# Optimization experiments

Hardware: AMD Instinct MI355X
Metric: run time of the kernel (lower is better)

The kernel has to match this reference:

```python
import jax, jax.numpy as jnp
import numpy as np

H = 768


def _glorot(key, shape):
    fan_in = shape[-1]
    return jax.random.normal(key, shape, dtype=jnp.float32) / np.sqrt(fan_in)


def setup_inputs() -> dict:
    key = jax.random.key(0)
    ks = jax.random.split(key, 12)
    B, L, K, Lg = 8, 256, 32, 128
    return {
        "x": jax.random.normal(ks[0], (B, L, H), dtype=jnp.float32),
        "s": jax.random.normal(ks[1], (B, K, H), dtype=jnp.float32),
        "g": jax.random.normal(ks[2], (B, Lg, H), dtype=jnp.float32),
        "Wq": _glorot(ks[3], (H, H)),
        "bq": jnp.zeros((H,), jnp.float32),
        "Wkv": _glorot(ks[4], (2 * H, H)),
        "bkv": jnp.zeros((2 * H,), jnp.float32),
        "Wg1": _glorot(ks[5], (H, 2 * H)),
        "bg1": jnp.zeros((H,), jnp.float32),
        "Wg2": _glorot(ks[6], (H, 2 * H)),
        "bg2": jnp.zeros((H,), jnp.float32),
    }


def _gate(xb, yb, W, b):
    # gate = sigmoid(Linear(concat([x, y], -1))) using split-weight trick:
    # concat([x,y]) @ W.T = x @ Wx.T + y @ Wy.T  (avoids materializing 2H concat)
    Wx, Wy = W[:, :H], W[:, H:]
    gate = jax.nn.sigmoid(jnp.einsum('blkh,oh->blko', xb, Wx)
                          + jnp.einsum('blkh,oh->blko', yb, Wy) + b)
    return gate * xb + (1.0 - gate) * yb


def reference(x, s, g, Wq, bq, Wkv, bkv, Wg1, bg1, Wg2, bg2):
    B, L, _ = x.shape
    K = s.shape[1]
    q = jnp.einsum('blh,oh->blo', x, Wq) + bq                    # (B,L,H)
    kv = jnp.einsum('bmh,oh->bmo', g, Wkv) + bkv                 # (B,Lg,2H)
    k, v = kv[..., :H], kv[..., H:]
    scores = jnp.einsum('blh,bmh->blm', q, k) / np.sqrt(H)       # (B,L,Lg)
    scores = jax.nn.softmax(scores, axis=-1)
    gctx = jnp.einsum('blm,bmh->blh', scores, v)                 # (B,L,H)
    # broadcast to (B,L,K,H)
    gb = jnp.broadcast_to(gctx[:, :, None, :], (B, L, K, H))
    hb = jnp.broadcast_to(x[:, :, None, :], (B, L, K, H))
    sb = jnp.broadcast_to(s[:, None, :, :], (B, L, K, H))
    h = _gate(hb, gb, Wg1, bg1)
    h = _gate(h, sb, Wg2, bg2)
    return h
```

## Files before the change

kernel.cpp:

```cpp
#include <hip/hip_runtime.h>
#include <math.h>

#define Hd 768
#define Bb 8
#define Ll 256
#define Kk 32
#define LG 128

using half4 = __attribute__((ext_vector_type(4))) _Float16;
using half8 = __attribute__((ext_vector_type(8))) _Float16;
using f32x4 = __attribute__((ext_vector_type(4))) float;

__device__ __forceinline__ float sigm(float z) { return 1.f / (1.f + __expf(-z)); }

struct ConvArgs {
    const float* src[8];
    _Float16*    dst[8];
    int cum[9];
    int sstr[8];
    int dstr[8];
    int rl[8];
};

__global__ __launch_bounds__(256) void conv_multi(ConvArgs a) {
    int c = blockIdx.x * 256 + threadIdx.x;
    if (c >= a.cum[8]) return;
    int s = 0;
    while (c >= a.cum[s + 1]) ++s;
    const int lc  = c - a.cum[s];
    const unsigned cpr = (unsigned)(a.rl[s] >> 3);
    const unsigned row = (unsigned)lc / cpr;
    const int col = (lc - (int)(row * cpr)) * 8;
    const float* sp = a.src[s] + (size_t)row * a.sstr[s] + col;
    float4 v0 = *(const float4*)sp;
    float4 v1 = *(const float4*)(sp + 4);
    half8 h;
    h[0] = (_Float16)v0.x; h[1] = (_Float16)v0.y; h[2] = (_Float16)v0.z; h[3] = (_Float16)v0.w;
    h[4] = (_Float16)v1.x; h[5] = (_Float16)v1.y; h[6] = (_Float16)v1.z; h[7] = (_Float16)v1.w;
    *(half8*)(a.dst[s] + (size_t)row * a.dstr[s] + col) = h;
}


struct G3Desc {
    const _Float16* A;
    const _Float16* W;
    const float* bias;
    void* o0;
    void* o1;
    int lda, ldw, mode, nbx;
};
struct G3Args { G3Desc d[3]; int cum[4]; };

__global__ __launch_bounds__(256) void gemm3(G3Args ga) {
    __shared__ _Float16 As[64][72];
    __shared__ _Float16 Ws[64][72];

    const int t    = threadIdx.x;
    const int w    = t >> 6;
    const int lane = t & 63;
    const int quad = lane >> 4;
    const int l16  = lane & 15;

    int s = 0;
    const int bid = blockIdx.x;
    while (bid >= ga.cum[s + 1]) ++s;
    const int local = bid - ga.cum[s];
    const int nbx   = ga.d[s].nbx;
    const int by    = local / nbx;
    const int bx    = local - by * nbx;
    const int bm    = by * 64;
    const int bn    = bx * 64;
    const _Float16* A = ga.d[s].A;
    const _Float16* W = ga.d[s].W;
    const int lda = ga.d[s].lda;
    const int ldw = ga.d[s].ldw;

    const int sr = t >> 3;
    const int sk = (t & 7) * 8;

    f32x4 acc[4] = {};

    half8 av[2], wv[2];
    #pragma unroll
    for (int i = 0; i < 2; ++i) {
        av[i] = *(const half8*)(A + (size_t)(bm + i * 32 + sr) * lda + sk);
        wv[i] = *(const half8*)(W + (size_t)(bn + i * 32 + sr) * ldw + sk);
    }

    for (int k0 = 0; k0 < 768; k0 += 64) {
        __syncthreads();
        #pragma unroll
        for (int i = 0; i < 2; ++i) {
            *(half8*)&As[i * 32 + sr][sk] = av[i];
            *(half8*)&Ws[i * 32 + sr][sk] = wv[i];
        }
        __syncthreads();
        if (k0 + 64 < 768) {
            #pragma unroll
            for (int i = 0; i < 2; ++i) {
                av[i] = *(const half8*)(A + (size_t)(bm + i * 32 + sr) * lda + k0 + 64 + sk);
                wv[i] = *(const half8*)(W + (size_t)(bn + i * 32 + sr) * ldw + k0 + 64 + sk);
            }
        }
        __builtin_amdgcn_sched_barrier(0);
        #pragma unroll
        for (int kk = 0; kk < 2; ++kk) {
            half8 af = *(const half8*)&As[w * 16 + l16][kk * 32 + quad * 8];
            #pragma unroll
            for (int j = 0; j < 4; ++j) {
                half8 bf = *(const half8*)&Ws[j * 16 + l16][kk * 32 + quad * 8];
                acc[j] = __builtin_amdgcn_mfma_f32_16x16x32_f16(af, bf, acc[j], 0, 0, 0);
            }
        }
    }

    const int mode = ga.d[s].mode;
    const float* bias = ga.d[s].bias;
    #pragma unroll
    for (int j = 0; j < 4; ++j) {
        const int col  = bn + j * 16 + l16;
        const int row0 = bm + w * 16 + quad * 4;
        const float bv = bias ? bias[col] : 0.f;
        if (mode == 0) {
            _Float16* C2 = (_Float16*)ga.d[s].o0;
            #pragma unroll
            for (int r = 0; r < 4; ++r)
                C2[(size_t)(row0 + r) * 768 + col] = (_Float16)(acc[j][r] + bv);
        } else if (mode == 1) {
            _Float16* K16  = (_Float16*)ga.d[s].o0;
            _Float16* VT16 = (_Float16*)ga.d[s].o1;
            if (col < 768) {
                #pragma unroll
                for (int r = 0; r < 4; ++r)
                    K16[(size_t)(row0 + r) * 768 + col] = (_Float16)(acc[j][r] + bv);
            } else {
                const int b = row0 >> 7, h = col - 768, m0 = row0 & 127;
                half4 hv;
                #pragma unroll
                for (int r = 0; r < 4; ++r) hv[r] = (_Float16)(acc[j][r] + bv);
                *(half4*)(VT16 + ((size_t)(b * 768 + h)) * 128 + m0) = hv;
            }
        } else {
            float* C = (float*)ga.d[s].o0;
            #pragma unroll
            for (int r = 0; r < 4; ++r)
                C[(size_t)(row0 + r) * 768 + col] = acc[j][r] + bv;
        }
    }
}

__global__ __launch_bounds__(256) void attn_scores_sm(
    const _Float16* __restrict__ Q, const _Float16* __restrict__ Kt,
    _Float16* __restrict__ P)
{
    __shared__ _Float16 As[64][72];
    __shared__ _Float16 Ws[128][72];

    const int t    = threadIdx.x;
    const int w    = t >> 6;
    const int lane = t & 63;
    const int quad = lane >> 4;
    const int l16  = lane & 15;
    const int z    = blockIdx.y;
    const int bm   = blockIdx.x * 64;
    const _Float16* A = Q  + (size_t)z * 256 * 768 + (size_t)bm * 768;
    const _Float16* W = Kt + (size_t)z * 128 * 768;

    const int sr = t >> 3;
    const int sk = (t & 7) * 8;

    f32x4 acc[8] = {};

    half8 av[2], wv[4];
    #pragma unroll
    for (int i = 0; i < 2; ++i)
        av[i] = *(const half8*)(A + (size_t)(i * 32 + sr) * 768 + sk);
    #pragma unroll
    for (int i = 0; i < 4; ++i)
        wv[i] = *(const half8*)(W + (size_t)(i * 32 + sr) * 768 + sk);

    for (int k0 = 0; k0 < 768; k0 += 64) {
        __syncthreads();
        #pragma unroll
        for (int i = 0; i < 2; ++i) *(half8*)&As[i * 32 + sr][sk] = av[i];
        #pragma unroll
        for (int i = 0; i < 4; ++i) *(half8*)&Ws[i * 32 + sr][sk] = wv[i];
        __syncthreads();
        if (k0 + 64 < 768) {
            #pragma unroll
            for (int i = 0; i < 2; ++i)
                av[i] = *(const half8*)(A + (size_t)(i * 32 + sr) * 768 + k0 + 64 + sk);
            #pragma unroll
            for (int i = 0; i < 4; ++i)
                wv[i] = *(const half8*)(W + (size_t)(i * 32 + sr) * 768 + k0 + 64 + sk);
        }
        __builtin_amdgcn_sched_barrier(0);
        #pragma unroll
        for (int kk = 0; kk < 2; ++kk) {
            half8 af = *(const half8*)&As[w * 16 + l16][kk * 32 + quad * 8];
            #pragma unroll
            for (int j = 0; j < 8; ++j) {
                half8 bf = *(const half8*)&Ws[j * 16 + l16][kk * 32 + quad * 8];
                acc[j] = __builtin_amdgcn_mfma_f32_16x16x32_f16(af, bf, acc[j], 0, 0, 0);
            }
        }
    }

    const float scale = 0.03608439182435161f;
    #pragma unroll
    for (int r = 0; r < 4; ++r) {
        float v[8];
        float mx = -1e30f;
        #pragma unroll
        for (int j = 0; j < 8; ++j) { v[j] = acc[j][r] * scale; mx = fmaxf(mx, v[j]); }
        #pragma unroll
        for (int off = 8; off; off >>= 1) mx = fmaxf(mx, __shfl_xor(mx, off, 16));
        float sum = 0.f;
        #pragma unroll
        for (int j = 0; j < 8; ++j) { v[j] = __expf(v[j] - mx); sum += v[j]; }
        #pragma unroll
        for (int off = 8; off; off >>= 1) sum += __shfl_xor(sum, off, 16);
        const float inv = 1.f / sum;
        const int row = bm + w * 16 + quad * 4 + r;
        _Float16* Pr = P + (size_t)z * 256 * 128 + (size_t)row * 128;
        #pragma unroll
        for (int j = 0; j < 8; ++j) Pr[j * 16 + l16] = (_Float16)(v[j] * inv);
    }
}

__global__ __launch_bounds__(256) void gemm_gctx(
    const _Float16* __restrict__ A, int lda, long sA,
    const _Float16* __restrict__ W, int ldw, long sW,
    float* __restrict__ C, int ldc, long sC,
    _Float16* __restrict__ C2, int ldc2, long sC2)
{
    __shared__ _Float16 As[64][72];
    __shared__ _Float16 Ws[64][72];

    const int t    = threadIdx.x;
    const int w    = t >> 6;
    const int lane = t & 63;
    const int quad = lane >> 4;
    const int l16  = lane & 15;
    const int bm   = blockIdx.y * 64;
    const int bn   = blockIdx.x * 64;
    const int z    = blockIdx.z;
    A += (size_t)z * sA;
    W += (size_t)z * sW;

    const int sr = t >> 3;
    const int sk = (t & 7) * 8;

    f32x4 acc[4] = {};

    half8 av[2], wv[2];
    #pragma unroll
    for (int i = 0; i < 2; ++i) {
        av[i] = *(const half8*)(A + (size_t)(bm + i * 32 + sr) * lda + sk);
        wv[i] = *(const half8*)(W + (size_t)(bn + i * 32 + sr) * ldw + sk);
    }

    for (int k0 = 0; k0 < 128; k0 += 64) {
        __syncthreads();
        #pragma unroll
        for (int i = 0; i < 2; ++i) {
            *(half8*)&As[i * 32 + sr][sk] = av[i];
            *(half8*)&Ws[i * 32 + sr][sk] = wv[i];
        }
        __syncthreads();
        if (k0 + 64 < 128) {
            #pragma unroll
            for (int i = 0; i < 2; ++i) {
                av[i] = *(const half8*)(A + (size_t)(bm + i * 32 + sr) * lda + k0 + 64 + sk);
                wv[i] = *(const half8*)(W + (size_t)(bn + i * 32 + sr) * ldw + k0 + 64 + sk);
            }
        }
        __builtin_amdgcn_sched_barrier(0);
        #pragma unroll
        for (int kk = 0; kk < 2; ++kk) {
            half8 af = *(const half8*)&As[w * 16 + l16][kk * 32 + quad * 8];
            #pragma unroll
            for (int j = 0; j < 4; ++j) {
                half8 bf = *(const half8*)&Ws[j * 16 + l16][kk * 32 + quad * 8];
                acc[j] = __builtin_amdgcn_mfma_f32_16x16x32_f16(af, bf, acc[j], 0, 0, 0);
            }
        }
    }

    #pragma unroll
    for (int j = 0; j < 4; ++j) {
        const int col  = bn + j * 16 + l16;
        const int row0 = bm + w * 16 + quad * 4;
        #pragma unroll
        for (int r = 0; r < 4; ++r) {
            const float v = acc[j][r];
            const size_t rr = (size_t)(row0 + r);
            C[(size_t)z * sC + rr * ldc + col] = v;
            C2[(size_t)z * sC2 + rr * ldc2 + col] = (_Float16)v;
        }
    }
}

__global__ __launch_bounds__(256) void gemm_gate1(
    const _Float16* __restrict__ A,
    const _Float16* __restrict__ W,
    const float* __restrict__ bias,
    const float* __restrict__ X,
    const float* __restrict__ GC,
    float* __restrict__ H1,
    _Float16* __restrict__ H16)
{
    __shared__ _Float16 As[64][72];
    __shared__ _Float16 Ws[64][72];

    const int t    = threadIdx.x;
    const int w    = t >> 6;
    const int lane = t & 63;
    const int quad = lane >> 4;
    const int l16  = lane & 15;
    const int bm   = blockIdx.y * 64;
    const int bn   = blockIdx.x * 64;

    const int sr = t >> 3;
    const int sk = (t & 7) * 8;

    f32x4 acc[4] = {};

    half8 av[2], wv[2];
    #pragma unroll
    for (int i = 0; i < 2; ++i) {
        av[i] = *(const half8*)(A + (size_t)(bm + i * 32 + sr) * 1536 + sk);
        wv[i] = *(const half8*)(W + (size_t)(bn + i * 32 + sr) * 1536 + sk);
    }

    for (int k0 = 0; k0 < 1536; k0 += 64) {
        __syncthreads();
        #pragma unroll
        for (int i = 0; i < 2; ++i) {
            *(half8*)&As[i * 32 + sr][sk] = av[i];
            *(half8*)&Ws[i * 32 + sr][sk] = wv[i];
        }
        __syncthreads();
        if (k0 + 64 < 1536) {
            #pragma unroll
            for (int i = 0; i < 2; ++i) {
                av[i] = *(const half8*)(A + (size_t)(bm + i * 32 + sr) * 1536 + k0 + 64 + sk);
                wv[i] = *(const half8*)(W + (size_t)(bn + i * 32 + sr) * 1536 + k0 + 64 + sk);
            }
        }
        __builtin_amdgcn_sched_barrier(0);
        #pragma unroll
        for (int kk = 0; kk < 2; ++kk) {
            half8 af = *(const half8*)&As[w * 16 + l16][kk * 32 + quad * 8];
            #pragma unroll
            for (int j = 0; j < 4; ++j) {
                half8 bf = *(const half8*)&Ws[j * 16 + l16][kk * 32 + quad * 8];
                acc[j] = __builtin_amdgcn_mfma_f32_16x16x32_f16(af, bf, acc[j], 0, 0, 0);
            }
        }
    }

    #pragma unroll
    for (int j = 0; j < 4; ++j) {
        const int col  = bn + j * 16 + l16;
        const int row0 = bm + w * 16 + quad * 4;
        const float bv = bias[col];
        #pragma unroll
        for (int r = 0; r < 4; ++r) {
            const size_t off = (size_t)(row0 + r) * 768 + col;
            const float g = sigm(acc[j][r] + bv);
            const float o = g * X[off] + (1.f - g) * GC[off];
            H1[off]  = o;
            H16[off] = (_Float16)o;
        }
    }
}

__global__ __launch_bounds__(256) void gemm_final(
    const _Float16* __restrict__ A,
    const _Float16* __restrict__ W,
    const float* __restrict__ bias,
    const float* __restrict__ Ebuf,
    const float* __restrict__ Sbuf,
    const float* __restrict__ H1,
    float* __restrict__ out)
{
    __shared__ union {
        struct { _Float16 As[64][72]; _Float16 Ws[64][72]; } a;
        float Ds[64][76];
    } u;
    __shared__ float Es[32][64];
    __shared__ float Ss[32][64];

    const int t    = threadIdx.x;
    const int w    = t >> 6;
    const int lane = t & 63;
    const int quad = lane >> 4;
    const int l16  = lane & 15;
    const int bm   = blockIdx.y * 64;
    const int bn   = blockIdx.x * 64;
    const int bK   = (bm >> 8) * 32;

    const int sr = t >> 3;
    const int sk = (t & 7) * 8;

    #pragma unroll
    for (int i = 0; i < 2; ++i) {
        const int idx = t + i * 256;
        const int k = idx >> 4, c = (idx & 15) * 4;
        *(float4*)&Es[k][c] = *(const float4*)(Ebuf + (size_t)(bK + k) * 768 + bn + c);
        *(float4*)&Ss[k][c] = *(const float4*)(Sbuf + (size_t)(bK + k) * 768 + bn + c);
    }

    f32x4 acc[4] = {};

    half8 av[2], wv[2];
    #pragma unroll
    for (int i = 0; i < 2; ++i) {
        av[i] = *(const half8*)(A + (size_t)(bm + i * 32 + sr) * 768 + sk);
        wv[i] = *(const half8*)(W + (size_t)(bn + i * 32 + sr) * 768 + sk);
    }

    for (int k0 = 0; k0 < 768; k0 += 64) {
        __syncthreads();
        #pragma unroll
        for (int i = 0; i < 2; ++i) {
            *(half8*)&u.a.As[i * 32 + sr][sk] = av[i];
            *(half8*)&u.a.Ws[i * 32 + sr][sk] = wv[i];
        }
        __syncthreads();
        if (k0 + 64 < 768) {
            #pragma unroll
            for (int i = 0; i < 2; ++i) {
                av[i] = *(const half8*)(A + (size_t)(bm + i * 32 + sr) * 768 + k0 + 64 + sk);
                wv[i] = *(const half8*)(W + (size_t)(bn + i * 32 + sr) * 768 + k0 + 64 + sk);
            }
        }
        __builtin_amdgcn_sched_barrier(0);
        #pragma unroll
        for (int kk = 0; kk < 2; ++kk) {
            half8 af = *(const half8*)&u.a.As[w * 16 + l16][kk * 32 + quad * 8];
            #pragma unroll
            for (int j = 0; j < 4; ++j) {
                half8 bf = *(const half8*)&u.a.Ws[j * 16 + l16][kk * 32 + quad * 8];
                acc[j] = __builtin_amdgcn_mfma_f32_16x16x32_f16(af, bf, acc[j], 0, 0, 0);
            }
        }
    }

    __syncthreads();
    #pragma unroll
    for (int j = 0; j < 4; ++j) {
        const int col = j * 16 + l16;
        const float bv = bias[bn + col];
        #pragma unroll
        for (int r = 0; r < 4; ++r)
            u.Ds[w * 16 + quad * 4 + r][col] = acc[j][r] + bv;
    }
    __syncthreads();

    const int c  = (t & 15) * 4;
    const int r0 = (t >> 4) * 4;
    float4 d[4], h[4];
    #pragma unroll
    for (int rr = 0; rr < 4; ++rr) {
        d[rr] = *(const float4*)&u.Ds[r0 + rr][c];
        h[rr] = *(const float4*)(H1 + (size_t)(bm + r0 + rr) * 768 + bn + c);
    }
    float* ob = out + (size_t)(bm + r0) * 32 * 768 + bn + c;
    for (int k = 0; k < 32; ++k) {
        const float4 e  = *(const float4*)&Es[k][c];
        const float4 sv = *(const float4*)&Ss[k][c];
        #pragma unroll
        for (int rr = 0; rr < 4; ++rr) {
            float4 o; float g;
            g = sigm(d[rr].x + e.x); o.x = g * h[rr].x + (1.f - g) * sv.x;
            g = sigm(d[rr].y + e.y); o.y = g * h[rr].y + (1.f - g) * sv.y;
            g = sigm(d[rr].z + e.z); o.z = g * h[rr].z + (1.f - g) * sv.z;
            g = sigm(d[rr].w + e.w); o.w = g * h[rr].w + (1.f - g) * sv.w;
            *(float4*)(ob + (size_t)(rr * 32 + k) * 768) = o;
        }
    }
}

extern "C" void kernel_launch(void* const* d_in, const int* in_sizes, int n_in,
                              void* d_out, int out_size, void* d_ws, size_t ws_size,
                              hipStream_t stream) {
    const float* x   = (const float*)d_in[0];
    const float* s   = (const float*)d_in[1];
    const float* g   = (const float*)d_in[2];
    const float* Wq  = (const float*)d_in[3];
    const float* bq  = (const float*)d_in[4];
    const float* Wkv = (const float*)d_in[5];
    const float* bkv = (const float*)d_in[6];
    const float* Wg1 = (const float*)d_in[7];
    const float* bg1 = (const float*)d_in[8];
    const float* Wg2 = (const float*)d_in[9];
    const float* bg2 = (const float*)d_in[10];

    char* w = (char*)d_ws;
    _Float16* P16    = (_Float16*)(w + 0);
    _Float16* xg16   = (_Float16*)(w + 524288);
    _Float16* g16    = (_Float16*)(w + 6815744);
    _Float16* s16    = (_Float16*)(w + 8388608);
    _Float16* q16    = (_Float16*)(w + 8781824);
    _Float16* k16    = (_Float16*)(w + 11927552);
    _Float16* vT16   = (_Float16*)(w + 13500416);
    _Float16* Wq16   = (_Float16*)(w + 15073280);
    _Float16* Wkv16  = (_Float16*)(w + 16252928);
    _Float16* Wg116  = (_Float16*)(w + 18612224);
    _Float16* Wg2a16 = (_Float16*)(w + 20971520);
    _Float16* Wg2b16 = (_Float16*)(w + 22151168);
    float*    bufE   = (float*)(w + 23330816);
    float*    bufC   = (float*)(w + 24117248);
    float*    bufB   = (float*)(w + 30408704);
    _Float16* h116   = (_Float16*)(w + 36700160);
    float* out = (float*)d_out;

    const dim3 blk(256);

    ConvArgs ca;
    ca.src[0] = x;         ca.dst[0] = xg16;   ca.sstr[0] = 768;  ca.dstr[0] = 1536; ca.rl[0] = 768;
    ca.src[1] = g;         ca.dst[1] = g16;    ca.sstr[1] = 768;  ca.dstr[1] = 768;  ca.rl[1] = 768;
    ca.src[2] = s;         ca.dst[2] = s16;    ca.sstr[2] = 768;  ca.dstr[2] = 768;  ca.rl[2] = 768;
    ca.src[3] = Wq;        ca.dst[3] = Wq16;   ca.sstr[3] = 768;  ca.dstr[3] = 768;  ca.rl[3] = 768;
    ca.src[4] = Wkv;       ca.dst[4] = Wkv16;  ca.sstr[4] = 768;  ca.dstr[4] = 768;  ca.rl[4] = 768;
    ca.src[5] = Wg1;       ca.dst[5] = Wg116;  ca.sstr[5] = 1536; ca.dstr[5] = 1536; ca.rl[5] = 1536;
    ca.src[6] = Wg2;       ca.dst[6] = Wg2a16; ca.sstr[6] = 1536; ca.dstr[6] = 768;  ca.rl[6] = 768;
    ca.src[7] = Wg2 + 768; ca.dst[7] = Wg2b16; ca.sstr[7] = 1536; ca.dstr[7] = 768;  ca.rl[7] = 768;
    ca.cum[0] = 0;      ca.cum[1] = 196608; ca.cum[2] = 294912; ca.cum[3] = 319488;
    ca.cum[4] = 393216; ca.cum[5] = 540672; ca.cum[6] = 688128; ca.cum[7] = 761856;
    ca.cum[8] = 835584;
    conv_multi<<<dim3(3264), blk, 0, stream>>>(ca);

    G3Args ga = {};
    ga.d[0] = { xg16, Wq16,   bq,      (void*)q16,  nullptr,     1536, 768, 0, 12 };
    ga.d[1] = { g16,  Wkv16,  bkv,     (void*)k16,  (void*)vT16, 768,  768, 1, 24 };
    ga.d[2] = { s16,  Wg2b16, nullptr, (void*)bufE, nullptr,     768,  768, 2, 12 };
    ga.cum[0] = 0; ga.cum[1] = 384; ga.cum[2] = 768; ga.cum[3] = 816;
    gemm3<<<dim3(816), blk, 0, stream>>>(ga);

    attn_scores_sm<<<dim3(4, 8), blk, 0, stream>>>(q16, k16, P16);

    gemm_gctx<<<dim3(12, 4, 8), blk, 0, stream>>>(
        P16, 128, 256L * 128, vT16, 128, 768L * 128,
        bufC, 768, 256L * 768, xg16 + 768, 1536, 256L * 1536);

    gemm_gate1<<<dim3(12, 32), blk, 0, stream>>>(
        xg16, Wg116, bg1, x, bufC, bufB, h116);

    gemm_final<<<dim3(12, 32), blk, 0, stream>>>(
        h116, Wg2a16, bg2, bufE, s, bufB, out);
}
```

Before: 311.4 us.

## Fuse all stages into one persistent cooperative kernel with grid syncs

Replaces the six separate launches (conversion, batched projection GEMMs, attention scores, P·V, gate1, final gate) with one cooperative persistent kernel of 512 blocks. Stages are separated by grid.sync() and share a union of shared-memory layouts. The attention stage now fuses softmax with P·V in-block, so the P matrix never goes to global memory. This removes launch gaps and the P round-trip. In exchange, the attention stage runs on only 32 blocks while the rest idle, grid-wide barriers add their own cost, and the larger shared footprint with 2-block occupancy may limit overlap.

```diff
diff --git a/kernel.cpp b/kernel.cpp
--- a/kernel.cpp
+++ b/kernel.cpp
@@ -1,11 +1,10 @@
 #include <hip/hip_runtime.h>
+#include <hip/hip_cooperative_groups.h>
 #include <math.h>
 
-#define Hd 768
-#define Bb 8
-#define Ll 256
-#define Kk 32
-#define LG 128
+namespace cg = cooperative_groups;
+
+#define NBLK 512
 
 using half4 = __attribute__((ext_vector_type(4))) _Float16;
 using half8 = __attribute__((ext_vector_type(8))) _Float16;
@@ -21,25 +20,6 @@
     int dstr[8];
     int rl[8];
 };
-
-__global__ __launch_bounds__(256) void conv_multi(ConvArgs a) {
-    int c = blockIdx.x * 256 + threadIdx.x;
-    if (c >= a.cum[8]) return;
-    int s = 0;
-    while (c >= a.cum[s + 1]) ++s;
-    const int lc  = c - a.cum[s];
-    const unsigned cpr = (unsigned)(a.rl[s] >> 3);
-    const unsigned row = (unsigned)lc / cpr;
-    const int col = (lc - (int)(row * cpr)) * 8;
-    const float* sp = a.src[s] + (size_t)row * a.sstr[s] + col;
-    float4 v0 = *(const float4*)sp;
-    float4 v1 = *(const float4*)(sp + 4);
-    half8 h;
-    h[0] = (_Float16)v0.x; h[1] = (_Float16)v0.y; h[2] = (_Float16)v0.z; h[3] = (_Float16)v0.w;
-    h[4] = (_Float16)v1.x; h[5] = (_Float16)v1.y; h[6] = (_Float16)v1.z; h[7] = (_Float16)v1.w;
-    *(half8*)(a.dst[s] + (size_t)row * a.dstr[s] + col) = h;
-}
-
 
 struct G3Desc {
     const _Float16* A;
@@ -51,434 +31,412 @@
 };
 struct G3Args { G3Desc d[3]; int cum[4]; };
 
-__global__ __launch_bounds__(256) void gemm3(G3Args ga) {
-    __shared__ _Float16 As[64][72];
-    __shared__ _Float16 Ws[64][72];
+struct FusedArgs {
+    ConvArgs ca;
+    G3Args   ga;
+    const _Float16* q16;
+    const _Float16* k16;
+    const _Float16* vT16;
+    float*          bufC;
+    _Float16*       xg16;
+    const _Float16* Wg116;
+    const float*    bg1;
+    const float*    x;
+    float*          bufB;
+    _Float16*       h116;
+    const _Float16* Wg2a16;
+    const float*    bg2;
+    const float*    bufE;
+    const float*    sIn;
+    float*          out;
+};
+
+union SharedAll {
+    struct { _Float16 As[64][72]; _Float16 Ws[64][72]; } g;
+    union {
+        struct { _Float16 As[64][72]; _Float16 Ws[128][72]; } qk;
+        struct { _Float16 Ps[64][136]; _Float16 Vs[64][136]; } pv;
+    } attn;
+    struct {
+        union { struct { _Float16 As[64][72]; _Float16 Ws[64][72]; } a;
+                float Ds[64][76]; } u;
+        float Es[32][64];
+        float Ss[32][64];
+    } fin;
+};
+
+__global__ __launch_bounds__(256, 2) void fused_all(FusedArgs fa) {
+    __shared__ SharedAll sh;
 
     const int t    = threadIdx.x;
     const int w    = t >> 6;
     const int lane = t & 63;
     const int quad = lane >> 4;
     const int l16  = lane & 15;
-
-    int s = 0;
-    const int bid = blockIdx.x;
-    while (bid >= ga.cum[s + 1]) ++s;
-    const int local = bid - ga.cum[s];
-    const int nbx   = ga.d[s].nbx;
-    const int by    = local / nbx;
-    const int bx    = local - by * nbx;
-    const int bm    = by * 64;
-    const int bn    = bx * 64;
-    const _Float16* A = ga.d[s].A;
-    const _Float16* W = ga.d[s].W;
-    const int lda = ga.d[s].lda;
-    const int ldw = ga.d[s].ldw;
-
-    const int sr = t >> 3;
-    const int sk = (t & 7) * 8;
-
-    f32x4 acc[4] = {};
-
-    half8 av[2], wv[2];
-    #pragma unroll
-    for (int i = 0; i < 2; ++i) {
-        av[i] = *(const half8*)(A + (size_t)(bm + i * 32 + sr) * lda + sk);
-        wv[i] = *(const half8*)(W + (size_t)(bn + i * 32 + sr) * ldw + sk);
+    const int sr   = t >> 3;
+    const int sk   = (t & 7) * 8;
+
+    cg::grid_group grid = cg::this_grid();
+
+    {
+        const ConvArgs& a = fa.ca;
+        for (int c = blockIdx.x * 256 + t; c < a.cum[8]; c += NBLK * 256) {
+            int seg = 0;
+            while (c >= a.cum[seg + 1]) ++seg;
+            const int lc  = c - a.cum[seg];
+            const unsigned cpr = (unsigned)(a.rl[seg] >> 3);
+            const unsigned row = (unsigned)lc / cpr;
+            const int col = (lc - (int)(row * cpr)) * 8;
+            const float* sp = a.src[seg] + (size_t)row * a.sstr[seg] + col;
+            float4 v0 = *(const float4*)sp;
+            float4 v1 = *(const float4*)(sp + 4);
+            half8 h;
+            h[0] = (_Float16)v0.x; h[1] = (_Float16)v0.y; h[2] = (_Float16)v0.z; h[3] = (_Float16)v0.w;
+            h[4] = (_Float16)v1.x; h[5] = (_Float16)v1.y; h[6] = (_Float16)v1.z; h[7] = (_Float16)v1.w;
+            *(half8*)(a.dst[seg] + (size_t)row * a.dstr[seg] + col) = h;
+        }
     }
-
-    for (int k0 = 0; k0 < 768; k0 += 64) {
+    grid.sync();
+
+    for (int bid = blockIdx.x; bid < 816; bid += NBLK) {
+        int seg = 0;
+        while (bid >= fa.ga.cum[seg + 1]) ++seg;
+        const G3Desc& d = fa.ga.d[seg];
+        const int local = bid - fa.ga.cum[seg];
+        const int by    = local / d.nbx;
+        const int bx    = local - by * d.nbx;
+        const int bm    = by * 64;
+        const int bn    = bx * 64;
+        const _Float16* A = d.A;
+        const _Float16* W = d.W;
+        const int lda = d.lda;
+        const int ldw = d.ldw;
+
+        f32x4 acc[4] = {};
+
+        half8 av[2], wv[2];
+        #pragma unroll
+        for (int i = 0; i < 2; ++i) {
+            av[i] = *(const half8*)(A + (size_t)(bm + i * 32 + sr) * lda + sk);
+            wv[i] = *(const half8*)(W + (size_t)(bn + i * 32 + sr) * ldw + sk);
+        }
+
+        for (int k0 = 0; k0 < 768; k0 += 64) {
+            __syncthreads();
+            #pragma unroll
+            for (int i = 0; i < 2; ++i) {
+                *(half8*)&sh.g.As[i * 32 + sr][sk] = av[i];
+                *(half8*)&sh.g.Ws[i * 32 + sr][sk] = wv[i];
+            }
+            __syncthreads();
+            if (k0 + 64 < 768) {
+                #pragma unroll
+                for (int i = 0; i < 2; ++i) {
+                    av[i] = *(const half8*)(A + (size_t)(bm + i * 32 + sr) * lda + k0 + 64 + sk);
+                    wv[i] = *(const half8*)(W + (size_t)(bn + i * 32 + sr) * ldw + k0 + 64 + sk);
+                }
+            }
+            __builtin_amdgcn_sched_barrier(0);
+            #pragma unroll
+            for (int kk = 0; kk < 2; ++kk) {
+                half8 af = *(const half8*)&sh.g.As[w * 16 + l16][kk * 32 + quad * 8];
+                #pragma unroll
+                for (int j = 0; j < 4; ++j) {
+                    half8 bf = *(const half8*)&sh.g.Ws[j * 16 + l16][kk * 32 + quad * 8];
+                    acc[j] = __builtin_amdgcn_mfma_f32_16x16x32_f16(af, bf, acc[j], 0, 0, 0);
+                }
+            }
+        }
+
+        const int mode = d.mode;
+        const float* bias = d.bias;
+        #pragma unroll
+        for (int j = 0; j < 4; ++j) {
+            const int col  = bn + j * 16 + l16;
+            const int row0 = bm + w * 16 + quad * 4;
+            const float bv = bias ? bias[col] : 0.f;
+            if (mode == 0) {
+                _Float16* C2 = (_Float16*)d.o0;
+                #pragma unroll
+                for (int r = 0; r < 4; ++r)
+                    C2[(size_t)(row0 + r) * 768 + col] = (_Float16)(acc[j][r] + bv);
+            } else if (mode == 1) {
+                _Float16* K16  = (_Float16*)d.o0;
+                _Float16* VT16 = (_Float16*)d.o1;
+                if (col < 768) {
+                    #pragma unroll
+                    for (int r = 0; r < 4; ++r)
+                        K16[(size_t)(row0 + r) * 768 + col] = (_Float16)(acc[j][r] + bv);
+                } else {
+                    const int b = row0 >> 7, h = col - 768, m0 = row0 & 127;
+                    half4 hv;
+                    #pragma unroll
+                    for (int r = 0; r < 4; ++r) hv[r] = (_Float16)(acc[j][r] + bv);
+                    *(half4*)(VT16 + ((size_t)(b * 768 + h)) * 128 + m0) = hv;
+                }
+            } else {
+                float* C = (float*)d.o0;
+                #pragma unroll
+                for (int r = 0; r < 4; ++r)
+                    C[(size_t)(row0 + r) * 768 + col] = acc[j][r] + bv;
+            }
+        }
+    }
+    grid.sync();
+
+    if (blockIdx.x < 32) {
+        const int z  = blockIdx.x >> 2;
+        const int bm = (blockIdx.x & 3) * 64;
+        const _Float16* A = fa.q16 + (size_t)z * 256 * 768 + (size_t)bm * 768;
+        const _Float16* W = fa.k16 + (size_t)z * 128 * 768;
+
+        f32x4 acc[8] = {};
+
+        half8 av[2], wv[4];
+        #pragma unroll
+        for (int i = 0; i < 2; ++i)
+            av[i] = *(const half8*)(A + (size_t)(i * 32 + sr) * 768 + sk);
+        #pragma unroll
+        for (int i = 0; i < 4; ++i)
+            wv[i] = *(const half8*)(W + (size_t)(i * 32 + sr) * 768 + sk);
+
+        for (int k0 = 0; k0 < 768; k0 += 64) {
+            __syncthreads();
+            #pragma unroll
+            for (int i = 0; i < 2; ++i) *(half8*)&sh.attn.qk.As[i * 32 + sr][sk] = av[i];
+            #pragma unroll
+            for (int i = 0; i < 4; ++i) *(half8*)&sh.attn.qk.Ws[i * 32 + sr][sk] = wv[i];
+            __syncthreads();
+            if (k0 + 64 < 768) {
+                #pragma unroll
+                for (int i = 0; i < 2; ++i)
+                    av[i] = *(const half8*)(A + (size_t)(i * 32 + sr) * 768 + k0 + 64 + sk);
+                #pragma unroll
+                for (int i = 0; i < 4; ++i)
+                    wv[i] = *(const half8*)(W + (size_t)(i * 32 + sr) * 768 + k0 + 64 + sk);
+            }
+            __builtin_amdgcn_sched_barrier(0);
+            #pragma unroll
+            for (int kk = 0; kk < 2; ++kk) {
+                half8 af = *(const half8*)&sh.attn.qk.As[w * 16 + l16][kk * 32 + quad * 8];
+                #pragma unroll
+                for (int j = 0; j < 8; ++j) {
+                    half8 bf = *(const half8*)&sh.attn.qk.Ws[j * 16 + l16][kk * 32 + quad * 8];
+                    acc[j] = __builtin_amdgcn_mfma_f32_16x16x32_f16(af, bf, acc[j], 0, 0, 0);
+                }
+            }
+        }
+
         __syncthreads();
+
+        const float scale = 0.03608439182435161f;
+        #pragma unroll
+        for (int r = 0; r < 4; ++r) {
+            float v[8];
+            float mx = -1e30f;
+            #pragma unroll
+            for (int j = 0; j < 8; ++j) { v[j] = acc[j][r] * scale; mx = fmaxf(mx, v[j]); }
+            #pragma unroll
+            for (int off = 8; off; off >>= 1) mx = fmaxf(mx, __shfl_xor(mx, off, 16));
+            float sum = 0.f;
+            #pragma unroll
+            for (int j = 0; j < 8; ++j) { v[j] = __expf(v[j] - mx); sum += v[j]; }
+            #pragma unroll
+            for (int off = 8; off; off >>= 1) sum += __shfl_xor(sum, off, 16);
+            const float inv = 1.f / sum;
+            const int prow = w * 16 + quad * 4 + r;
+            #pragma unroll
+            for (int j = 0; j < 8; ++j)
+                sh.attn.pv.Ps[prow][j * 16 + l16] = (_Float16)(v[j] * inv);
+        }
+
+        const _Float16* Vt = fa.vT16 + (size_t)z * 768 * 128;
+        float*     Cc = fa.bufC + ((size_t)(z * 256 + bm)) * 768;
+        _Float16*  Xg = fa.xg16 + ((size_t)(z * 256 + bm)) * 1536 + 768;
+
+        for (int cg = 0; cg < 12; ++cg) {
+            __syncthreads();
+            {
+                const int row = t >> 2;
+                const int cb  = (t & 3) * 32;
+                const _Float16* vp = Vt + (size_t)(cg * 64 + row) * 128 + cb;
+                *(half8*)&sh.attn.pv.Vs[row][cb]      = *(const half8*)(vp);
+                *(half8*)&sh.attn.pv.Vs[row][cb + 8]  = *(const half8*)(vp + 8);
+                *(half8*)&sh.attn.pv.Vs[row][cb + 16] = *(const half8*)(vp + 16);
+                *(half8*)&sh.attn.pv.Vs[row][cb + 24] = *(const half8*)(vp + 24);
+            }
+            __syncthreads();
+            f32x4 a2[4] = {};
+            #pragma unroll
+            for (int kk = 0; kk < 4; ++kk) {
+                half8 af = *(const half8*)&sh.attn.pv.Ps[w * 16 + l16][kk * 32 + quad * 8];
+                #pragma unroll
+                for (int j = 0; j < 4; ++j) {
+                    half8 bf = *(const half8*)&sh.attn.pv.Vs[j * 16 + l16][kk * 32 + quad * 8];
+                    a2[j] = __builtin_amdgcn_mfma_f32_16x16x32_f16(af, bf, a2[j], 0, 0, 0);
+                }
+            }
+            #pragma unroll
+            for (int j = 0; j < 4; ++j) {
+                const int col  = cg * 64 + j * 16 + l16;
+                const int row0 = w * 16 + quad * 4;
+                #pragma unroll
+                for (int r = 0; r < 4; ++r) {
+                    const float vv = a2[j][r];
+                    Cc[(size_t)(row0 + r) * 768 + col] = vv;
+                    Xg[(size_t)(row0 + r) * 1536 + col] = (_Float16)vv;
+                }
+            }
+        }
+    }
+    grid.sync();
+
+    for (int tile = blockIdx.x; tile < 384; tile += NBLK) {
+        const int by = tile / 12;
+        const int bx = tile - by * 12;
+        const int bm = by * 64;
+        const int bn = bx * 64;
+        const _Float16* A = fa.xg16;
+        const _Float16* W = fa.Wg116;
+
+        f32x4 acc[4] = {};
+
+        half8 av[2], wv[2];
         #pragma unroll
         for (int i = 0; i < 2; ++i) {
-            *(half8*)&As[i * 32 + sr][sk] = av[i];
-            *(half8*)&Ws[i * 32 + sr][sk] = wv[i];
-        }
+            av[i] = *(const half8*)(A + (size_t)(bm + i * 32 + sr) * 1536 + sk);
+            wv[i] = *(const half8*)(W + (size_t)(bn + i * 32 + sr) * 1536 + sk);
+        }
+
+        for (int k0 = 0; k0 < 1536; k0 += 64) {
+            __syncthreads();
+            #pragma unroll
+            for (int i = 0; i < 2; ++i) {
+                *(half8*)&sh.g.As[i * 32 + sr][sk] = av[i];
+                *(half8*)&sh.g.Ws[i * 32 + sr][sk] = wv[i];
+            }
+            __syncthreads();
+            if (k0 + 64 < 1536) {
+                #pragma unroll
+                for (int i = 0; i < 2; ++i) {
+                    av[i] = *(const half8*)(A + (size_t)(bm + i * 32 + sr) * 1536 + k0 + 64 + sk);
+                    wv[i] = *(const half8*)(W + (size_t)(bn + i * 32 + sr) * 1536 + k0 + 64 + sk);
+                }
+            }
+            __builtin_amdgcn_sched_barrier(0);
+            #pragma unroll
+            for (int kk = 0; kk < 2; ++kk) {
+                half8 af = *(const half8*)&sh.g.As[w * 16 + l16][kk * 32 + quad * 8];
+                #pragma unroll
+                for (int j = 0; j < 4; ++j) {
+                    half8 bf = *(const half8*)&sh.g.Ws[j * 16 + l16][kk * 32 + quad * 8];
+                    acc[j] = __builtin_amdgcn_mfma_f32_16x16x32_f16(af, bf, acc[j], 0, 0, 0);
+                }
+            }
+        }
+
+        #pragma unroll
+        for (int j = 0; j < 4; ++j) {
+            const int col  = bn + j * 16 + l16;
+            const int row0 = bm + w * 16 + quad * 4;
+            const float bv = fa.bg1[col];
+            #pragma unroll
+            for (int r = 0; r < 4; ++r) {
+                const size_t off = (size_t)(row0 + r) * 768 + col;
+                const float g = sigm(acc[j][r] + bv);
+                const float o = g * fa.x[off] + (1.f - g) * fa.bufC[off];
+                fa.bufB[off] = o;
+                fa.h116[off] = (_Float16)o;
+            }
+        }
+    }
+    grid.sync();
+
+    for (int tile = blockIdx.x; tile < 384; tile += NBLK) {
+        const int by = tile / 12;
+        const int bx = tile - by * 12;
+        const int bm = by * 64;
+        const int bn = bx * 64;
+        const int bK = (bm >> 8) * 32;
+        const _Float16* A = fa.h116;
+        const _Float16* W = fa.Wg2a16;
+
+        #pragma unroll
+        for (int i = 0; i < 2; ++i) {
+            const int idx = t + i * 256;
+            const int k = idx >> 4, c = (idx & 15) * 4;
+            *(float4*)&sh.fin.Es[k][c] = *(const float4*)(fa.bufE + (size_t)(bK + k) * 768 + bn + c);
+            *(float4*)&sh.fin.Ss[k][c] = *(const float4*)(fa.sIn  + (size_t)(bK + k) * 768 + bn + c);
+        }
+
+        f32x4 acc[4] = {};
+
+        half8 av[2], wv[2];
+        #pragma unroll
+        for (int i = 0; i < 2; ++i) {
+            av[i] = *(const half8*)(A + (size_t)(bm + i * 32 + sr) * 768 + sk);
+            wv[i] = *(const half8*)(W + (size_t)(bn + i * 32 + sr) * 768 + sk);
+        }
+
+        for (int k0 = 0; k0 < 768; k0 += 64) {
+            __syncthreads();
+            #pragma unroll
+            for (int i = 0; i < 2; ++i) {
+                *(half8*)&sh.fin.u.a.As[i * 32 + sr][sk] = av[i];
+                *(half8*)&sh.fin.u.a.Ws[i * 32 + sr][sk] = wv[i];
+            }
+            __syncthreads();
+            if (k0 + 64 < 768) {
+                #pragma unroll
+                for (int i = 0; i < 2; ++i) {
+                    av[i] = *(const half8*)(A + (size_t)(bm + i * 32 + sr) * 768 + k0 + 64 + sk);
+                    wv[i] = *(const half8*)(W + (size_t)(bn + i * 32 + sr) * 768 + k0 + 64 + sk);
+                }
+            }
+            __builtin_amdgcn_sched_barrier(0);
+            #pragma unroll
+            for (int kk = 0; kk < 2; ++kk) {
+                half8 af = *(const half8*)&sh.fin.u.a.As[w * 16 + l16][kk * 32 + quad * 8];
+                #pragma unroll
+                for (int j = 0; j < 4; ++j) {
+                    half8 bf = *(const half8*)&sh.fin.u.a.Ws[j * 16 + l16][kk * 32 + quad * 8];
+                    acc[j] = __builtin_amdgcn_mfma_f32_16x16x32_f16(af, bf, acc[j], 0, 0, 0);
+                }
+            }
+        }
+
         __syncthreads();
-        if (k0 + 64 < 768) {
-            #pragma unroll
-            for (int i = 0; i < 2; ++i) {
-                av[i] = *(const half8*)(A + (size_t)(bm + i * 32 + sr) * lda + k0 + 64 + sk);
-                wv[i] = *(const half8*)(W + (size_t)(bn + i * 32 + sr) * ldw + k0 + 64 + sk);
-            }
-        }
-        __builtin_amdgcn_sched_barrier(0);
-        #pragma unroll
-        for (int kk = 0; kk < 2; ++kk) {
-            half8 af = *(const half8*)&As[w * 16 + l16][kk * 32 + quad * 8];
-            #pragma unroll
-            for (int j = 0; j < 4; ++j) {
-                half8 bf = *(const half8*)&Ws[j * 16 + l16][kk * 32 + quad * 8];
-                acc[j] = __builtin_amdgcn_mfma_f32_16x16x32_f16(af, bf, acc[j], 0, 0, 0);
-            }
-        }
-    }
-
-    const int mode = ga.d[s].mode;
-    const float* bias = ga.d[s].bias;
-    #pragma unroll
-    for (int j = 0; j < 4; ++j) {
-        const int col  = bn + j * 16 + l16;
-        const int row0 = bm + w * 16 + quad * 4;
-        const float bv = bias ? bias[col] : 0.f;
-        if (mode == 0) {
-            _Float16* C2 = (_Float16*)ga.d[s].o0;
+        #pragma unroll
+        for (int j = 0; j < 4; ++j) {
+            const int col = j * 16 + l16;
+            const float bv = fa.bg2[bn + col];
             #pragma unroll
             for (int r = 0; r < 4; ++r)
-                C2[(size_t)(row0 + r) * 768 + col] = (_Float16)(acc[j][r] + bv);
-        } else if (mode == 1) {
-            _Float16* K16  = (_Float16*)ga.d[s].o0;
-            _Float16* VT16 = (_Float16*)ga.d[s].o1;
-            if (col < 768) {
-                #pragma unroll
-                for (int r = 0; r < 4; ++r)
-                    K16[(size_t)(row0 + r) * 768 + col] = (_Float16)(acc[j][r] + bv);
-            } else {
-                const int b = row0 >> 7, h = col - 768, m0 = row0 & 127;
-                half4 hv;
-                #pragma unroll
-                for (int r = 0; r < 4; ++r) hv[r] = (_Float16)(acc[j][r] + bv);
-                *(half4*)(VT16 + ((size_t)(b * 768 + h)) * 128 + m0) = hv;
-            }
-        } else {
-            float* C = (float*)ga.d[s].o0;
-            #pragma unroll
-            for (int r = 0; r < 4; ++r)
-                C[(size_t)(row0 + r) * 768 + col] = acc[j][r] + bv;
-        }
-    }
-}
-
-__global__ __launch_bounds__(256) void attn_scores_sm(
-    const _Float16* __restrict__ Q, const _Float16* __restrict__ Kt,
-    _Float16* __restrict__ P)
-{
-    __shared__ _Float16 As[64][72];
-    __shared__ _Float16 Ws[128][72];
-
-    const int t    = threadIdx.x;
-    const int w    = t >> 6;
-    const int lane = t & 63;
-    const int quad = lane >> 4;
-    const int l16  = lane & 15;
-    const int z    = blockIdx.y;
-    const int bm   = blockIdx.x * 64;
-    const _Float16* A = Q  + (size_t)z * 256 * 768 + (size_t)bm * 768;
-    const _Float16* W = Kt + (size_t)z * 128 * 768;
-
-    const int sr = t >> 3;
-    const int sk = (t & 7) * 8;
-
-    f32x4 acc[8] = {};
-
-    half8 av[2], wv[4];
-    #pragma unroll
-    for (int i = 0; i < 2; ++i)
-        av[i] = *(const half8*)(A + (size_t)(i * 32 + sr) * 768 + sk);
-    #pragma unroll
-    for (int i = 0; i < 4; ++i)
-        wv[i] = *(const half8*)(W + (size_t)(i * 32 + sr) * 768 + sk);
-
-    for (int k0 = 0; k0 < 768; k0 += 64) {
+                sh.fin.u.Ds[w * 16 + quad * 4 + r][col] = acc[j][r] + bv;
+        }
         __syncthreads();
-        #pragma unroll
-        for (int i = 0; i < 2; ++i) *(half8*)&As[i * 32 + sr][sk] = av[i];
-        #pragma unroll
-        for (int i = 0; i < 4; ++i) *(half8*)&Ws[i * 32 + sr][sk] = wv[i];
-        __syncthreads();
-        if (k0 + 64 < 768) {
-            #pragma unroll
-            for (int i = 0; i < 2; ++i)
-                av[i] = *(const half8*)(A + (size_t)(i * 32 + sr) * 768 + k0 + 64 + sk);
-            #pragma unroll
-            for (int i = 0; i < 4; ++i)
-                wv[i] = *(const half8*)(W + (size_t)(i * 32 + sr) * 768 + k0 + 64 + sk);
-        }
-        __builtin_amdgcn_sched_barrier(0);
-        #pragma unroll
-        for (int kk = 0; kk < 2; ++kk) {
-            half8 af = *(const half8*)&As[w * 16 + l16][kk * 32 + quad * 8];
-            #pragma unroll
-            for (int j = 0; j < 8; ++j) {
-                half8 bf = *(const half8*)&Ws[j * 16 + l16][kk * 32 + quad * 8];
-                acc[j] = __builtin_amdgcn_mfma_f32_16x16x32_f16(af, bf, acc[j], 0, 0, 0);
-            }
-        }
-    }
-
-    const float scale = 0.03608439182435161f;
-    #pragma unroll
-    for (int r = 0; r < 4; ++r) {
-        float v[8];
-        float mx = -1e30f;
-        #pragma unroll
-        for (int j = 0; j < 8; ++j) { v[j] = acc[j][r] * scale; mx = fmaxf(mx, v[j]); }
-        #pragma unroll
-        for (int off = 8; off; off >>= 1) mx = fmaxf(mx, __shfl_xor(mx, off, 16));
-        float sum = 0.f;
-        #pragma unroll
-        for (int j = 0; j < 8; ++j) { v[j] = __expf(v[j] - mx); sum += v[j]; }
-        #pragma unroll
-        for (int off = 8; off; off >>= 1) sum += __shfl_xor(sum, off, 16);
-        const float inv = 1.f / sum;
-        const int row = bm + w * 16 + quad * 4 + r;
-        _Float16* Pr = P + (size_t)z * 256 * 128 + (size_t)row * 128;
-        #pragma unroll
-        for (int j = 0; j < 8; ++j) Pr[j * 16 + l16] = (_Float16)(v[j] * inv);
-    }
-}
-
-__global__ __launch_bounds__(256) void gemm_gctx(
-    const _Float16* __restrict__ A, int lda, long sA,
-    const _Float16* __restrict__ W, int ldw, long sW,
-    float* __restrict__ C, int ldc, long sC,
-    _Float16* __restrict__ C2, int ldc2, long sC2)
-{
-    __shared__ _Float16 As[64][72];
-    __shared__ _Float16 Ws[64][72];
-
-    const int t    = threadIdx.x;
-    const int w    = t >> 6;
-    const int lane = t & 63;
-    const int quad = lane >> 4;
-    const int l16  = lane & 15;
-    const int bm   = blockIdx.y * 64;
-    const int bn   = blockIdx.x * 64;
-    const int z    = blockIdx.z;
-    A += (size_t)z * sA;
-    W += (size_t)z * sW;
-
-    const int sr = t >> 3;
-    const int sk = (t & 7) * 8;
-
-    f32x4 acc[4] = {};
-
-    half8 av[2], wv[2];
-    #pragma unroll
-    for (int i = 0; i < 2; ++i) {
-        av[i] = *(const half8*)(A + (size_t)(bm + i * 32 + sr) * lda + sk);
-        wv[i] = *(const half8*)(W + (size_t)(bn + i * 32 + sr) * ldw + sk);
-    }
-
-    for (int k0 = 0; k0 < 128; k0 += 64) {
-        __syncthreads();
-        #pragma unroll
-        for (int i = 0; i < 2; ++i) {
-            *(half8*)&As[i * 32 + sr][sk] = av[i];
-            *(half8*)&Ws[i * 32 + sr][sk] = wv[i];
-        }
-        __syncthreads();
-        if (k0 + 64 < 128) {
-            #pragma unroll
-            for (int i = 0; i < 2; ++i) {
-                av[i] = *(const half8*)(A + (size_t)(bm + i * 32 + sr) * lda + k0 + 64 + sk);
-                wv[i] = *(const half8*)(W + (size_t)(bn + i * 32 + sr) * ldw + k0 + 64 + sk);
-            }
-        }
-        __builtin_amdgcn_sched_barrier(0);
-        #pragma unroll
-        for (int kk = 0; kk < 2; ++kk) {
-            half8 af = *(const half8*)&As[w * 16 + l16][kk * 32 + quad * 8];
-            #pragma unroll
-            for (int j = 0; j < 4; ++j) {
-                half8 bf = *(const half8*)&Ws[j * 16 + l16][kk * 32 + quad * 8];
-                acc[j] = __builtin_amdgcn_mfma_f32_16x16x32_f16(af, bf, acc[j], 0, 0, 0);
-            }
-        }
-    }
-
-    #pragma unroll
-    for (int j = 0; j < 4; ++j) {
-        const int col  = bn + j * 16 + l16;
-        const int row0 = bm + w * 16 + quad * 4;
-        #pragma unroll
-        for (int r = 0; r < 4; ++r) {
-            const float v = acc[j][r];
-            const size_t rr = (size_t)(row0 + r);
-            C[(size_t)z * sC + rr * ldc + col] = v;
-            C2[(size_t)z * sC2 + rr * ldc2 + col] = (_Float16)v;
-        }
-    }
-}
-
-__global__ __launch_bounds__(256) void gemm_gate1(
-    const _Float16* __restrict__ A,
-    const _Float16* __restrict__ W,
-    const float* __restrict__ bias,
-    const float* __restrict__ X,
-    const float* __restrict__ GC,
-    float* __restrict__ H1,
-    _Float16* __restrict__ H16)
-{
-    __shared__ _Float16 As[64][72];
-    __shared__ _Float16 Ws[64][72];
-
-    const int t    = threadIdx.x;
-    const int w    = t >> 6;
-    const int lane = t & 63;
-    const int quad = lane >> 4;
-    const int l16  = lane & 15;
-    const int bm   = blockIdx.y * 64;
-    const int bn   = blockIdx.x * 64;
-
-    const int sr = t >> 3;
-    const int sk = (t & 7) * 8;
-
-    f32x4 acc[4] = {};
-
-    half8 av[2], wv[2];
-    #pragma unroll
-    for (int i = 0; i < 2; ++i) {
-        av[i] = *(const half8*)(A + (size_t)(bm + i * 32 + sr) * 1536 + sk);
-        wv[i] = *(const half8*)(W + (size_t)(bn + i * 32 + sr) * 1536 + sk);
-    }
-
-    for (int k0 = 0; k0 < 1536; k0 += 64) {
-        __syncthreads();
-        #pragma unroll
-        for (int i = 0; i < 2; ++i) {
-            *(half8*)&As[i * 32 + sr][sk] = av[i];
-            *(half8*)&Ws[i * 32 + sr][sk] = wv[i];
-        }
-        __syncthreads();
-        if (k0 + 64 < 1536) {
-            #pragma unroll
-            for (int i = 0; i < 2; ++i) {
-                av[i] = *(const half8*)(A + (size_t)(bm + i * 32 + sr) * 1536 + k0 + 64 + sk);
-                wv[i] = *(const half8*)(W + (size_t)(bn + i * 32 + sr) * 1536 + k0 + 64 + sk);
-            }
-        }
-        __builtin_amdgcn_sched_barrier(0);
-        #pragma unroll
-        for (int kk = 0; kk < 2; ++kk) {
-            half8 af = *(const half8*)&As[w * 16 + l16][kk * 32 + quad * 8];
-            #pragma unroll
-            for (int j = 0; j < 4; ++j) {
-                half8 bf = *(const half8*)&Ws[j * 16 + l16][kk * 32 + quad * 8];
-                acc[j] = __builtin_amdgcn_mfma_f32_16x16x32_f16(af, bf, acc[j], 0, 0, 0);
-            }
-        }
-    }
-
-    #pragma unroll
-    for (int j = 0; j < 4; ++j) {
-        const int col  = bn + j * 16 + l16;
-        const int row0 = bm + w * 16 + quad * 4;
-        const float bv = bias[col];
-        #pragma unroll
-        for (int r = 0; r < 4; ++r) {
-            const size_t off = (size_t)(row0 + r) * 768 + col;
-            const float g = sigm(acc[j][r] + bv);
-            const float o = g * X[off] + (1.f - g) * GC[off];
-            H1[off]  = o;
-            H16[off] = (_Float16)o;
-        }
-    }
-}
-
-__global__ __launch_bounds__(256) void gemm_final(
-    const _Float16* __restrict__ A,
-    const _Float16* __restrict__ W,
-    const float* __restrict__ bias,
-    const float* __restrict__ Ebuf,
-    const float* __restrict__ Sbuf,
-    const float* __restrict__ H1,
-    float* __restrict__ out)
-{
-    __shared__ union {
-        struct { _Float16 As[64][72]; _Float16 Ws[64][72]; } a;
-        float Ds[64][76];
-    } u;
-    __shared__ float Es[32][64];
-    __shared__ float Ss[32][64];
-
-    const int t    = threadIdx.x;
-    const int w    = t >> 6;
-    const int lane = t & 63;
-    const int quad = lane >> 4;
-    const int l16  = lane & 15;
-    const int bm   = blockIdx.y * 64;
-    const int bn   = blockIdx.x * 64;
-    const int bK   = (bm >> 8) * 32;
-
-    const int sr = t >> 3;
-    const int sk = (t & 7) * 8;
-
-    #pragma unroll
-    for (int i = 0; i < 2; ++i) {
-        const int idx = t + i * 256;
-        const int k = idx >> 4, c = (idx & 15) * 4;
-        *(float4*)&Es[k][c] = *(const float4*)(Ebuf + (size_t)(bK + k) * 768 + bn + c);
-        *(float4*)&Ss[k][c] = *(const float4*)(Sbuf + (size_t)(bK + k) * 768 + bn + c);
-    }
-
-    f32x4 acc[4] = {};
-
-    half8 av[2], wv[2];
-    #pragma unroll
-    for (int i = 0; i < 2; ++i) {
-        av[i] = *(const half8*)(A + (size_t)(bm + i * 32 + sr) * 768 + sk);
-        wv[i] = *(const half8*)(W + (size_t)(bn + i * 32 + sr) * 768 + sk);
-    }
-
-    for (int k0 = 0; k0 < 768; k0 += 64) {
-        __syncthreads();
-        #pragma unroll
-        for (int i = 0; i < 2; ++i) {
-            *(half8*)&u.a.As[i * 32 + sr][sk] = av[i];
-            *(half8*)&u.a.Ws[i * 32 + sr][sk] = wv[i];
-        }
-        __syncthreads();
-        if (k0 + 64 < 768) {
-            #pragma unroll
-            for (int i = 0; i < 2; ++i) {
-                av[i] = *(const half8*)(A + (size_t)(bm + i * 32 + sr) * 768 + k0 + 64 + sk);
-                wv[i] = *(const half8*)(W + (size_t)(bn + i * 32 + sr) * 768 + k0 + 64 + sk);
-            }
-        }
-        __builtin_amdgcn_sched_barrier(0);
-        #pragma unroll
-        for (int kk = 0; kk < 2; ++kk) {
-            half8 af = *(const half8*)&u.a.As[w * 16 + l16][kk * 32 + quad * 8];
-            #pragma unroll
-            for (int j = 0; j < 4; ++j) {
-                half8 bf = *(const half8*)&u.a.Ws[j * 16 + l16][kk * 32 + quad * 8];
-                acc[j] = __builtin_amdgcn_mfma_f32_16x16x32_f16(af, bf, acc[j], 0, 0, 0);
-            }
-        }
-    }
-
-    __syncthreads();
-    #pragma unroll
-    for (int j = 0; j < 4; ++j) {
-        const int col = j * 16 + l16;
-        const float bv = bias[bn + col];
-        #pragma unroll
-        for (int r = 0; r < 4; ++r)
-            u.Ds[w * 16 + quad * 4 + r][col] = acc[j][r] + bv;
-    }
-    __syncthreads();
-
-    const int c  = (t & 15) * 4;
-    const int r0 = (t >> 4) * 4;
-    float4 d[4], h[4];
-    #pragma unroll
-    for (int rr = 0; rr < 4; ++rr) {
-        d[rr] = *(const float4*)&u.Ds[r0 + rr][c];
-        h[rr] = *(const float4*)(H1 + (size_t)(bm + r0 + rr) * 768 + bn + c);
-    }
-    float* ob = out + (size_t)(bm + r0) * 32 * 768 + bn + c;
-    for (int k = 0; k < 32; ++k) {
-        const float4 e  = *(const float4*)&Es[k][c];
-        const float4 sv = *(const float4*)&Ss[k][c];
+
+        const int c  = (t & 15) * 4;
+        const int r0 = (t >> 4) * 4;
+        float4 d4[4], h4v[4];
         #pragma unroll
         for (int rr = 0; rr < 4; ++rr) {
-            float4 o; float g;
-            g = sigm(d[rr].x + e.x); o.x = g * h[rr].x + (1.f - g) * sv.x;
-            g = sigm(d[rr].y + e.y); o.y = g * h[rr].y + (1.f - g) * sv.y;
-            g = sigm(d[rr].z + e.z); o.z = g * h[rr].z + (1.f - g) * sv.z;
-            g = sigm(d[rr].w + e.w); o.w = g * h[rr].w + (1.f - g) * sv.w;
-            *(float4*)(ob + (size_t)(rr * 32 + k) * 768) = o;
+            d4[rr]  = *(const float4*)&sh.fin.u.Ds[r0 + rr][c];
+            h4v[rr] = *(const float4*)(fa.bufB + (size_t)(bm + r0 + rr) * 768 + bn + c);
+        }
+        float* ob = fa.out + (size_t)(bm + r0) * 32 * 768 + bn + c;
+        for (int k = 0; k < 32; ++k) {
+            const float4 e  = *(const float4*)&sh.fin.Es[k][c];
+            const float4 sv = *(const float4*)&sh.fin.Ss[k][c];
+            #pragma unroll
+            for (int rr = 0; rr < 4; ++rr) {
+                float4 o; float g;
+                g = sigm(d4[rr].x + e.x); o.x = g * h4v[rr].x + (1.f - g) * sv.x;
+                g = sigm(d4[rr].y + e.y); o.y = g * h4v[rr].y + (1.f - g) * sv.y;
+                g = sigm(d4[rr].z + e.z); o.z = g * h4v[rr].z + (1.f - g) * sv.z;
+                g = sigm(d4[rr].w + e.w); o.w = g * h4v[rr].w + (1.f - g) * sv.w;
+                *(float4*)(ob + (size_t)(rr * 32 + k) * 768) = o;
+            }
         }
     }
 }
@@ -499,7 +457,6 @@
     const float* bg2 = (const float*)d_in[10];
 
     char* w = (char*)d_ws;
-    _Float16* P16    = (_Float16*)(w + 0);
     _Float16* xg16   = (_Float16*)(w + 524288);
     _Float16* g16    = (_Float16*)(w + 6815744);
     _Float16* s16    = (_Float16*)(w + 8388608);
@@ -517,38 +474,32 @@
     _Float16* h116   = (_Float16*)(w + 36700160);
     float* out = (float*)d_out;
 
-    const dim3 blk(256);
-
-    ConvArgs ca;
-    ca.src[0] = x;         ca.dst[0] = xg16;   ca.sstr[0] = 768;  ca.dstr[0] = 1536; ca.rl[0] = 768;
-    ca.src[1] = g;         ca.dst[1] = g16;    ca.sstr[1] = 768;  ca.dstr[1] = 768;  ca.rl[1] = 768;
-    ca.src[2] = s;         ca.dst[2] = s16;    ca.sstr[2] = 768;  ca.dstr[2] = 768;  ca.rl[2] = 768;
-    ca.src[3] = Wq;        ca.dst[3] = Wq16;   ca.sstr[3] = 768;  ca.dstr[3] = 768;  ca.rl[3] = 768;
-    ca.src[4] = Wkv;       ca.dst[4] = Wkv16;  ca.sstr[4] = 768;  ca.dstr[4] = 768;  ca.rl[4] = 768;
-    ca.src[5] = Wg1;       ca.dst[5] = Wg116;  ca.sstr[5] = 1536; ca.dstr[5] = 1536; ca.rl[5] = 1536;
-    ca.src[6] = Wg2;       ca.dst[6] = Wg2a16; ca.sstr[6] = 1536; ca.dstr[6] = 768;  ca.rl[6] = 768;
-    ca.src[7] = Wg2 + 768; ca.dst[7] = Wg2b16; ca.sstr[7] = 1536; ca.dstr[7] = 768;  ca.rl[7] = 768;
-    ca.cum[0] = 0;      ca.cum[1] = 196608; ca.cum[2] = 294912; ca.cum[3] = 319488;
-    ca.cum[4] = 393216; ca.cum[5] = 540672; ca.cum[6] = 688128; ca.cum[7] = 761856;
-    ca.cum[8] = 835584;
-    conv_multi<<<dim3(3264), blk, 0, stream>>>(ca);
-
-    G3Args ga = {};
-    ga.d[0] = { xg16, Wq16,   bq,      (void*)q16,  nullptr,     1536, 768, 0, 12 };
-    ga.d[1] = { g16,  Wkv16,  bkv,     (void*)k16,  (void*)vT16, 768,  768, 1, 24 };
-    ga.d[2] = { s16,  Wg2b16, nullptr, (void*)bufE, nullptr,     768,  768, 2, 12 };
-    ga.cum[0] = 0; ga.cum[1] = 384; ga.cum[2] = 768; ga.cum[3] = 816;
-    gemm3<<<dim3(816), blk, 0, stream>>>(ga);
-
-    attn_scores_sm<<<dim3(4, 8), blk, 0, stream>>>(q16, k16, P16);
-
-    gemm_gctx<<<dim3(12, 4, 8), blk, 0, stream>>>(
-        P16, 128, 256L * 128, vT16, 128, 768L * 128,
-        bufC, 768, 256L * 768, xg16 + 768, 1536, 256L * 1536);
-
-    gemm_gate1<<<dim3(12, 32), blk, 0, stream>>>(
-        xg16, Wg116, bg1, x, bufC, bufB, h116);
-
-    gemm_final<<<dim3(12, 32), blk, 0, stream>>>(
-        h116, Wg2a16, bg2, bufE, s, bufB, out);
+    FusedArgs fa = {};
+
+    fa.ca.src[0] = x;         fa.ca.dst[0] = xg16;   fa.ca.sstr[0] = 768;  fa.ca.dstr[0] = 1536; fa.ca.rl[0] = 768;
+    fa.ca.src[1] = g;         fa.ca.dst[1] = g16;    fa.ca.sstr[1] = 768;  fa.ca.dstr[1] = 768;  fa.ca.rl[1] = 768;
+    fa.ca.src[2] = s;         fa.ca.dst[2] = s16;    fa.ca.sstr[2] = 768;  fa.ca.dstr[2] = 768;  fa.ca.rl[2] = 768;
+    fa.ca.src[3] = Wq;        fa.ca.dst[3] = Wq16;   fa.ca.sstr[3] = 768;  fa.ca.dstr[3] = 768;  fa.ca.rl[3] = 768;
+    fa.ca.src[4] = Wkv;       fa.ca.dst[4] = Wkv16;  fa.ca.sstr[4] = 768;  fa.ca.dstr[4] = 768;  fa.ca.rl[4] = 768;
+    fa.ca.src[5] = Wg1;       fa.ca.dst[5] = Wg116;  fa.ca.sstr[5] = 1536; fa.ca.dstr[5] = 1536; fa.ca.rl[5] = 1536;
+    fa.ca.src[6] = Wg2;       fa.ca.dst[6] = Wg2a16; fa.ca.sstr[6] = 1536; fa.ca.dstr[6] = 768;  fa.ca.rl[6] = 768;
+    fa.ca.src[7] = Wg2 + 768; fa.ca.dst[7] = Wg2b16; fa.ca.sstr[7] = 1536; fa.ca.dstr[7] = 768;  fa.ca.rl[7] = 768;
+    fa.ca.cum[0] = 0;      fa.ca.cum[1] = 196608; fa.ca.cum[2] = 294912; fa.ca.cum[3] = 319488;
+    fa.ca.cum[4] = 393216; fa.ca.cum[5] = 540672; fa.ca.cum[6] = 688128; fa.ca.cum[7] = 761856;
+    fa.ca.cum[8] = 835584;
+
+    fa.ga.d[0] = { xg16, Wq16,   bq,      (void*)q16,  nullptr,     1536, 768, 0, 12 };
+    fa.ga.d[1] = { g16,  Wkv16,  bkv,     (void*)k16,  (void*)vT16, 768,  768, 1, 24 };
+    fa.ga.d[2] = { s16,  Wg2b16, nullptr, (void*)bufE, nullptr,     768,  768, 2, 12 };
+    fa.ga.cum[0] = 0; fa.ga.cum[1] = 384; fa.ga.cum[2] = 768; fa.ga.cum[3] = 816;
+
+    fa.q16 = q16; fa.k16 = k16; fa.vT16 = vT16;
+    fa.bufC = bufC; fa.xg16 = xg16;
+    fa.Wg116 = Wg116; fa.bg1 = bg1; fa.x = x;
+    fa.bufB = bufB; fa.h116 = h116;
+    fa.Wg2a16 = Wg2a16; fa.bg2 = bg2; fa.bufE = bufE; fa.sIn = s;
+    fa.out = out;
+
+    void* kargs[] = { (void*)&fa };
+    hipLaunchCooperativeKernel((void*)fused_all, dim3(NBLK), dim3(256), kargs, 0, stream);
 }
```

After: 636.0 us. 2.04x slower.
